# Kernel optimization log

Measured on AMD Instinct MI355X. Metric: run time of the kernel, lower is better.

The kernel has to match this reference:

```python
import jax, jax.numpy as jnp
import numpy as np
from math import sqrt


def setup_inputs() -> dict:
    key = jax.random.key(0)
    kq, kk, kv = jax.random.split(key, 3)
    B, L, H, E = 4, 2048, 8, 64
    S, D = L, E
    return {
        "queries": jax.random.normal(kq, (B, L, H, E), dtype=jnp.float32),
        "keys": jax.random.normal(kk, (B, S, H, E), dtype=jnp.float32),
        "values": jax.random.normal(kv, (B, S, H, D), dtype=jnp.float32),
    }


def reference(queries, keys, values):
    # FullAttention with mask_flag=True (TriangularCausalMask), dropout p=0,
    # output_attention=False. scale = 1/sqrt(E).
    B, L, H, E = queries.shape
    S = keys.shape[1]
    scale = 1.0 / sqrt(E)
    # scores: [B, H, L, S]
    scores = jnp.einsum("blhe,bshe->bhls", queries, keys)
    # causal mask: positions s > l are masked (upper triangle above diagonal)
    causal = jnp.tril(jnp.ones((L, S), dtype=bool))  # True = keep
    neg_inf = jnp.finfo(scores.dtype).min
    scores = jnp.where(causal, scores, neg_inf)
    A = jax.nn.softmax(scale * scores, axis=-1)  # [B,H,L,S]
    # context: [B, L, H, D]
    V = jnp.einsum("bhls,bshd->blhd", A, values)
    return V
```

## Files before the change

kernel.cpp:

```cpp
#include <hip/hip_runtime.h>
#include <math.h>

#define BD 4
#define LD 2048
#define HD 8
#define ED 64
#define TQ 64
#define TK 64
#define RS (HD * ED)

typedef __attribute__((ext_vector_type(8))) _Float16 f16x8;
typedef __attribute__((ext_vector_type(4))) _Float16 f16x4;
typedef __attribute__((ext_vector_type(4))) float f32x4;
typedef __attribute__((ext_vector_type(4))) unsigned int u32x4;
typedef __attribute__((ext_vector_type(2))) unsigned int u32x2;
typedef unsigned int u32;
typedef unsigned long long u64;

__device__ inline u32 pkh(float a, float b) {
    return __builtin_bit_cast(u32, __builtin_amdgcn_cvt_pkrtz(a, b));
}
__device__ inline u64 pkh4(float a, float b, float c, float d) {
    return (u64)pkh(a, b) | ((u64)pkh(c, d) << 32);
}
__device__ inline int swz(int row, int bcol) {
    return row * 128 + ((((bcol >> 4) ^ row) & 7) << 4) + (bcol & 15);
}

__global__ __launch_bounds__(256, 4)
void fa_mfma_q64(const float* __restrict__ Q, const float* __restrict__ K,
                 const float* __restrict__ V, float* __restrict__ O) {
    __shared__ __align__(16) char smem[32768];

    const int t    = threadIdx.x;
    const int lane = t & 63;
    const int w    = t >> 6;
    const int m16  = lane & 15;
    const int quad = lane >> 4;

    const int b = blockIdx.x >> 3;
    const int h = blockIdx.x & 7;
    const int y  = (int)blockIdx.y;
    const int r  = y & 7;
    const int c  = y >> 3;
    const int qt = (c == 0) ? (31 - r) : (c == 1) ? (r + 8)
                 : (c == 2) ? (23 - r) : r;
    const int q0  = qt * TQ;
    const int len = qt + 1;

    const int ks  = t >> 2;
    const int ke0 = (t & 3) << 2;
    const int vs0 = (t & 15) << 2;
    const int vd0 = (t >> 4) << 2;

    const float* Kbase = K + ((size_t)((b * LD + ks) * HD + h)) * ED + ke0;
    const float* Vbase = V + ((size_t)((b * LD + vs0) * HD + h)) * ED + vd0;

    const float qscale = 0.125f * 1.44269504088896340736f;
    f16x8 qf[2];
    {
        const float* qrow =
            Q + ((size_t)((b * LD + q0 + (w << 4) + m16) * HD + h)) * ED;
        #pragma unroll
        for (int hf = 0; hf < 2; ++hf) {
            const float4 x  = *(const float4*)(qrow + hf * 32 + quad * 8);
            const float4 y4 = *(const float4*)(qrow + hf * 32 + quad * 8 + 4);
            u32x4 p;
            p[0] = pkh(x.x * qscale, x.y * qscale);
            p[1] = pkh(x.z * qscale, x.w * qscale);
            p[2] = pkh(y4.x * qscale, y4.y * qscale);
            p[3] = pkh(y4.z * qscale, y4.w * qscale);
            qf[hf] = __builtin_bit_cast(f16x8, p);
        }
    }

    f32x4 oacc[4];
    float l_i = 0.0f;
    #pragma unroll
    for (int nt = 0; nt < 4; ++nt) oacc[nt] = (f32x4){0.f, 0.f, 0.f, 0.f};

    float4 kx[4], vx[4];
    {
        #pragma unroll
        for (int j = 0; j < 4; ++j) kx[j] = *(const float4*)(Kbase + 16 * j);
        #pragma unroll
        for (int rr = 0; rr < 4; ++rr) vx[rr] = *(const float4*)(Vbase + rr * RS);
        char* wK = smem;
        char* wV = smem + 16384;
        #pragma unroll
        for (int j = 0; j < 4; ++j)
            *(u64*)(wK + swz(ks, 2 * (ke0 + 16 * j))) = pkh4(kx[j].x, kx[j].y, kx[j].z, kx[j].w);
        *(u64*)(wV + swz(vd0 + 0, 2 * vs0)) = pkh4(vx[0].x, vx[1].x, vx[2].x, vx[3].x);
        *(u64*)(wV + swz(vd0 + 1, 2 * vs0)) = pkh4(vx[0].y, vx[1].y, vx[2].y, vx[3].y);
        *(u64*)(wV + swz(vd0 + 2, 2 * vs0)) = pkh4(vx[0].z, vx[1].z, vx[2].z, vx[3].z);
        *(u64*)(wV + swz(vd0 + 3, 2 * vs0)) = pkh4(vx[0].w, vx[1].w, vx[2].w, vx[3].w);
    }
    __syncthreads();

    for (int kt = 0; kt < len; ++kt) {
        char* rK = smem + ((kt & 1) << 13);
        char* rV = smem + 16384 + ((kt & 1) << 13);
        const bool pre = kt < len - 1;

        if (pre) {
            const float* kp = Kbase + (size_t)(kt + 1) * (TK * RS);
            const float* vp = Vbase + (size_t)(kt + 1) * (TK * RS);
            #pragma unroll
            for (int j = 0; j < 4; ++j) kx[j] = *(const float4*)(kp + 16 * j);
            #pragma unroll
            for (int rr = 0; rr < 4; ++rr) vx[rr] = *(const float4*)(vp + rr * RS);
        }

        f32x4 sacc[4];
        #pragma unroll
        for (int kc = 0; kc < 4; ++kc) {
            const f16x8 kf0 = *(const f16x8*)(rK + swz(kc * 16 + m16, quad * 16));
            const f16x8 kf1 = *(const f16x8*)(rK + swz(kc * 16 + m16, 64 + quad * 16));
            f32x4 z = {0.f, 0.f, 0.f, 0.f};
            z = __builtin_amdgcn_mfma_f32_16x16x32_f16(kf0, qf[0], z, 0, 0, 0);
            z = __builtin_amdgcn_mfma_f32_16x16x32_f16(kf1, qf[1], z, 0, 0, 0);
            sacc[kc] = z;
        }

        if (kt == qt) {
            const int ql = (w << 4) + m16;
            #pragma unroll
            for (int kc = 0; kc < 4; ++kc)
                #pragma unroll
                for (int i = 0; i < 4; ++i)
                    if (kc * 16 + quad * 4 + i > ql) sacc[kc][i] = -INFINITY;
        }

        f16x4 pf[4];
        #pragma unroll
        for (int kc = 0; kc < 4; ++kc) {
            float p0 = __builtin_amdgcn_exp2f(sacc[kc][0]);
            float p1 = __builtin_amdgcn_exp2f(sacc[kc][1]);
            float p2 = __builtin_amdgcn_exp2f(sacc[kc][2]);
            float p3 = __builtin_amdgcn_exp2f(sacc[kc][3]);
            l_i += (p0 + p1) + (p2 + p3);
            u32x2 pp;
            pp[0] = pkh(p0, p1);
            pp[1] = pkh(p2, p3);
            pf[kc] = __builtin_bit_cast(f16x4, pp);
        }

        #pragma unroll
        for (int kc = 0; kc < 4; ++kc) {
            #pragma unroll
            for (int dt = 0; dt < 4; ++dt) {
                const f16x4 vf = *(const f16x4*)
                    (rV + swz(dt * 16 + m16, 2 * (kc * 16 + quad * 4)));
                oacc[dt] = __builtin_amdgcn_mfma_f32_16x16x16f16(vf, pf[kc], oacc[dt], 0, 0, 0);
            }
        }

        if (pre) {
            char* wK = smem + ((kt & 1) ? 0 : 8192);
            char* wV = smem + 16384 + ((kt & 1) ? 0 : 8192);
            #pragma unroll
            for (int j = 0; j < 4; ++j)
                *(u64*)(wK + swz(ks, 2 * (ke0 + 16 * j))) = pkh4(kx[j].x, kx[j].y, kx[j].z, kx[j].w);
            *(u64*)(wV + swz(vd0 + 0, 2 * vs0)) = pkh4(vx[0].x, vx[1].x, vx[2].x, vx[3].x);
            *(u64*)(wV + swz(vd0 + 1, 2 * vs0)) = pkh4(vx[0].y, vx[1].y, vx[2].y, vx[3].y);
            *(u64*)(wV + swz(vd0 + 2, 2 * vs0)) = pkh4(vx[0].z, vx[1].z, vx[2].z, vx[3].z);
            *(u64*)(wV + swz(vd0 + 3, 2 * vs0)) = pkh4(vx[0].w, vx[1].w, vx[2].w, vx[3].w);
        }
        __syncthreads();
    }

    {
        float l = l_i;
        l += __shfl_xor(l, 16);
        l += __shfl_xor(l, 32);
        const float inv = 1.0f / l;
        float* orow =
            O + ((size_t)((b * LD + q0 + (w << 4) + m16) * HD + h)) * ED;
        #pragma unroll
        for (int dt = 0; dt < 4; ++dt) {
            float4 o;
            o.x = oacc[dt][0] * inv;
            o.y = oacc[dt][1] * inv;
            o.z = oacc[dt][2] * inv;
            o.w = oacc[dt][3] * inv;
            *(float4*)(orow + dt * 16 + quad * 4) = o;
        }
    }
}

extern "C" void kernel_launch(void* const* d_in, const int* in_sizes, int n_in,
                              void* d_out, int out_size, void* d_ws, size_t ws_size,
                              hipStream_t stream) {
    const float* Q = (const float*)d_in[0];
    const float* K = (const float*)d_in[1];
    const float* V = (const float*)d_in[2];
    float* O = (float*)d_out;
    dim3 grid(BD * HD, 32);
    fa_mfma_q64<<<grid, 256, 0, stream>>>(Q, K, V, O);
}
```

Baseline: 124.0 us.

## Fold paired causal query tiles into one block for balanced work

Each block now processes two query tiles, f and 31-f, back to back in a single 33-iteration key loop, so every block does the same amount of causal work. The grid is halved to 512 blocks, which removes tail imbalance and halves per-block launch and prologue costs. The trade-off is fewer blocks in flight on a large GPU and longer serial chains per block, plus mid-loop output writes and Q reloads. The kt sequence for the second tile runs backwards, so the diagonal mask is applied at its first tile.

```diff
diff --git a/kernel.cpp b/kernel.cpp
--- a/kernel.cpp
+++ b/kernel.cpp
@@ -28,8 +28,8 @@
 }
 
 __global__ __launch_bounds__(256, 4)
-void fa_mfma_q64(const float* __restrict__ Q, const float* __restrict__ K,
-                 const float* __restrict__ V, float* __restrict__ O) {
+void fa_mfma_fold(const float* __restrict__ Q, const float* __restrict__ K,
+                  const float* __restrict__ V, float* __restrict__ O) {
     __shared__ __align__(16) char smem[32768];
 
     const int t    = threadIdx.x;
@@ -40,13 +40,9 @@
 
     const int b = blockIdx.x >> 3;
     const int h = blockIdx.x & 7;
-    const int y  = (int)blockIdx.y;
-    const int r  = y & 7;
-    const int c  = y >> 3;
-    const int qt = (c == 0) ? (31 - r) : (c == 1) ? (r + 8)
-                 : (c == 2) ? (23 - r) : r;
-    const int q0  = qt * TQ;
-    const int len = qt + 1;
+    const int f = (int)blockIdx.y;
+    const int qtA = f;
+    const int qtB = 31 - f;
 
     const int ks  = t >> 2;
     const int ke0 = (t & 3) << 2;
@@ -60,7 +56,7 @@
     f16x8 qf[2];
     {
         const float* qrow =
-            Q + ((size_t)((b * LD + q0 + (w << 4) + m16) * HD + h)) * ED;
+            Q + ((size_t)((b * LD + qtA * TQ + (w << 4) + m16) * HD + h)) * ED;
         #pragma unroll
         for (int hf = 0; hf < 2; ++hf) {
             const float4 x  = *(const float4*)(qrow + hf * 32 + quad * 8);
@@ -97,14 +93,17 @@
     }
     __syncthreads();
 
-    for (int kt = 0; kt < len; ++kt) {
-        char* rK = smem + ((kt & 1) << 13);
-        char* rV = smem + 16384 + ((kt & 1) << 13);
-        const bool pre = kt < len - 1;
+    for (int i = 0; i < 33; ++i) {
+        const int kt = (i <= f) ? i : 32 - i;
+        const int qt = (i <= f) ? qtA : qtB;
+        char* rK = smem + ((i & 1) << 13);
+        char* rV = smem + 16384 + ((i & 1) << 13);
+        const bool pre = i < 32;
 
         if (pre) {
-            const float* kp = Kbase + (size_t)(kt + 1) * (TK * RS);
-            const float* vp = Vbase + (size_t)(kt + 1) * (TK * RS);
+            const int ktn = (i < f) ? (i + 1) : (31 - i);
+            const float* kp = Kbase + (size_t)ktn * (TK * RS);
+            const float* vp = Vbase + (size_t)ktn * (TK * RS);
             #pragma unroll
             for (int j = 0; j < 4; ++j) kx[j] = *(const float4*)(kp + 16 * j);
             #pragma unroll
@@ -127,8 +126,8 @@
             #pragma unroll
             for (int kc = 0; kc < 4; ++kc)
                 #pragma unroll
-                for (int i = 0; i < 4; ++i)
-                    if (kc * 16 + quad * 4 + i > ql) sacc[kc][i] = -INFINITY;
+                for (int ii = 0; ii < 4; ++ii)
+                    if (kc * 16 + quad * 4 + ii > ql) sacc[kc][ii] = -INFINITY;
         }
 
         f16x4 pf[4];
@@ -155,9 +154,42 @@
             }
         }
 
+        if (i == f) {
+            float l = l_i;
+            l += __shfl_xor(l, 16);
+            l += __shfl_xor(l, 32);
+            const float inv = 1.0f / l;
+            float* orow =
+                O + ((size_t)((b * LD + qtA * TQ + (w << 4) + m16) * HD + h)) * ED;
+            #pragma unroll
+            for (int dt = 0; dt < 4; ++dt) {
+                float4 o;
+                o.x = oacc[dt][0] * inv;
+                o.y = oacc[dt][1] * inv;
+                o.z = oacc[dt][2] * inv;
+                o.w = oacc[dt][3] * inv;
+                *(float4*)(orow + dt * 16 + quad * 4) = o;
+                oacc[dt] = (f32x4){0.f, 0.f, 0.f, 0.f};
+            }
+            l_i = 0.0f;
+            const float* qrow =
+                Q + ((size_t)((b * LD + qtB * TQ + (w << 4) + m16) * HD + h)) * ED;
+            #pragma unroll
+            for (int hf = 0; hf < 2; ++hf) {
+                const float4 x  = *(const float4*)(qrow + hf * 32 + quad * 8);
+                const float4 y4 = *(const float4*)(qrow + hf * 32 + quad * 8 + 4);
+                u32x4 p;
+                p[0] = pkh(x.x * qscale, x.y * qscale);
+                p[1] = pkh(x.z * qscale, x.w * qscale);
+                p[2] = pkh(y4.x * qscale, y4.y * qscale);
+                p[3] = pkh(y4.z * qscale, y4.w * qscale);
+                qf[hf] = __builtin_bit_cast(f16x8, p);
+            }
+        }
+
         if (pre) {
-            char* wK = smem + ((kt & 1) ? 0 : 8192);
-            char* wV = smem + 16384 + ((kt & 1) ? 0 : 8192);
+            char* wK = smem + ((i & 1) ? 0 : 8192);
+            char* wV = smem + 16384 + ((i & 1) ? 0 : 8192);
             #pragma unroll
             for (int j = 0; j < 4; ++j)
                 *(u64*)(wK + swz(ks, 2 * (ke0 + 16 * j))) = pkh4(kx[j].x, kx[j].y, kx[j].z, kx[j].w);
@@ -175,7 +207,7 @@
         l += __shfl_xor(l, 32);
         const float inv = 1.0f / l;
         float* orow =
-            O + ((size_t)((b * LD + q0 + (w << 4) + m16) * HD + h)) * ED;
+            O + ((size_t)((b * LD + qtB * TQ + (w << 4) + m16) * HD + h)) * ED;
         #pragma unroll
         for (int dt = 0; dt < 4; ++dt) {
             float4 o;
@@ -195,6 +227,6 @@
     const float* K = (const float*)d_in[1];
     const float* V = (const float*)d_in[2];
     float* O = (float*)d_out;
-    dim3 grid(BD * HD, 32);
-    fa_mfma_q64<<<grid, 256, 0, stream>>>(Q, K, V, O);
-}
+    dim3 grid(BD * HD, 16);
+    fa_mfma_fold<<<grid, 256, 0, stream>>>(Q, K, V, O);
+}
```

New measurement: 128.1 us. 3.3% more time.

## Precompute swizzled fp16 K/V tiles and stream them via global_load_lds

Applied to the files above, without the earlier changes.

Adds a pre-pass kernel that converts K and V to fp16 once, in the final swizzled/transposed LDS layout, and stores them in workspace. The attention kernel then copies those tiles straight into LDS with global_load_lds, with no per-block fp32 loads, conversion or LDS stores. This removes the redundant conversion that every query-tile block repeated and halves the bytes read per K/V tile. The cost is an extra launch plus a workspace round trip. The old path remains as a fallback when the workspace is too small.

```diff
diff --git a/kernel.cpp b/kernel.cpp
--- a/kernel.cpp
+++ b/kernel.cpp
@@ -8,6 +8,8 @@
 #define TQ 64
 #define TK 64
 #define RS (HD * ED)
+#define NT 32
+#define TILE_BYTES 8192
 
 typedef __attribute__((ext_vector_type(8))) _Float16 f16x8;
 typedef __attribute__((ext_vector_type(4))) _Float16 f16x4;
@@ -26,10 +28,50 @@
 __device__ inline int swz(int row, int bcol) {
     return row * 128 + ((((bcol >> 4) ^ row) & 7) << 4) + (bcol & 15);
 }
+__device__ __forceinline__ void gload_lds16(const char* g, char* l) {
+    __builtin_amdgcn_global_load_lds(
+        (const __attribute__((address_space(1))) unsigned int*)g,
+        (__attribute__((address_space(3))) unsigned int*)l, 16, 0, 0);
+}
 
 __global__ __launch_bounds__(256, 4)
-void fa_mfma_q64(const float* __restrict__ Q, const float* __restrict__ K,
-                 const float* __restrict__ V, float* __restrict__ O) {
+void cvt_kv(const float* __restrict__ K, const float* __restrict__ V,
+            char* __restrict__ Kimg, char* __restrict__ Vimg) {
+    const int t  = threadIdx.x;
+    const int b  = blockIdx.x >> 3;
+    const int h  = blockIdx.x & 7;
+    const int kt = blockIdx.y;
+
+    const int ks  = t >> 2;
+    const int ke0 = (t & 3) << 2;
+    const int vs0 = (t & 15) << 2;
+    const int vd0 = (t >> 4) << 2;
+
+    const size_t tb = ((size_t)((b * HD + h) * NT + kt)) * TILE_BYTES;
+    char* kd = Kimg + tb;
+    char* vd = Vimg + tb;
+
+    const float* kp = K + ((size_t)((b * LD + kt * TK + ks) * HD + h)) * ED + ke0;
+    const float* vp = V + ((size_t)((b * LD + kt * TK + vs0) * HD + h)) * ED + vd0;
+
+    float4 kx[4], vx[4];
+    #pragma unroll
+    for (int j = 0; j < 4; ++j) kx[j] = *(const float4*)(kp + 16 * j);
+    #pragma unroll
+    for (int r = 0; r < 4; ++r) vx[r] = *(const float4*)(vp + r * RS);
+
+    #pragma unroll
+    for (int j = 0; j < 4; ++j)
+        *(u64*)(kd + swz(ks, 2 * (ke0 + 16 * j))) = pkh4(kx[j].x, kx[j].y, kx[j].z, kx[j].w);
+    *(u64*)(vd + swz(vd0 + 0, 2 * vs0)) = pkh4(vx[0].x, vx[1].x, vx[2].x, vx[3].x);
+    *(u64*)(vd + swz(vd0 + 1, 2 * vs0)) = pkh4(vx[0].y, vx[1].y, vx[2].y, vx[3].y);
+    *(u64*)(vd + swz(vd0 + 2, 2 * vs0)) = pkh4(vx[0].z, vx[1].z, vx[2].z, vx[3].z);
+    *(u64*)(vd + swz(vd0 + 3, 2 * vs0)) = pkh4(vx[0].w, vx[1].w, vx[2].w, vx[3].w);
+}
+
+__global__ __launch_bounds__(256, 4)
+void fa_f16img(const char* __restrict__ Kimg, const char* __restrict__ Vimg,
+               const float* __restrict__ Q, float* __restrict__ O) {
     __shared__ __align__(16) char smem[32768];
 
     const int t    = threadIdx.x;
@@ -48,13 +90,10 @@
     const int q0  = qt * TQ;
     const int len = qt + 1;
 
-    const int ks  = t >> 2;
-    const int ke0 = (t & 3) << 2;
-    const int vs0 = (t & 15) << 2;
-    const int vd0 = (t >> 4) << 2;
-
-    const float* Kbase = K + ((size_t)((b * LD + ks) * HD + h)) * ED + ke0;
-    const float* Vbase = V + ((size_t)((b * LD + vs0) * HD + h)) * ED + vd0;
+    const char* Kt = Kimg + (size_t)(b * HD + h) * NT * TILE_BYTES;
+    const char* Vt = Vimg + (size_t)(b * HD + h) * NT * TILE_BYTES;
+    const int lsrc = (w << 10) + (lane << 4);
+    const int ldst = (w << 10);
 
     const float qscale = 0.125f * 1.44269504088896340736f;
     f16x8 qf[2];
@@ -79,36 +118,30 @@
     #pragma unroll
     for (int nt = 0; nt < 4; ++nt) oacc[nt] = (f32x4){0.f, 0.f, 0.f, 0.f};
 
-    float4 kx[4], vx[4];
-    {
-        #pragma unroll
-        for (int j = 0; j < 4; ++j) kx[j] = *(const float4*)(Kbase + 16 * j);
-        #pragma unroll
-        for (int rr = 0; rr < 4; ++rr) vx[rr] = *(const float4*)(Vbase + rr * RS);
-        char* wK = smem;
-        char* wV = smem + 16384;
-        #pragma unroll
-        for (int j = 0; j < 4; ++j)
-            *(u64*)(wK + swz(ks, 2 * (ke0 + 16 * j))) = pkh4(kx[j].x, kx[j].y, kx[j].z, kx[j].w);
-        *(u64*)(wV + swz(vd0 + 0, 2 * vs0)) = pkh4(vx[0].x, vx[1].x, vx[2].x, vx[3].x);
-        *(u64*)(wV + swz(vd0 + 1, 2 * vs0)) = pkh4(vx[0].y, vx[1].y, vx[2].y, vx[3].y);
-        *(u64*)(wV + swz(vd0 + 2, 2 * vs0)) = pkh4(vx[0].z, vx[1].z, vx[2].z, vx[3].z);
-        *(u64*)(wV + swz(vd0 + 3, 2 * vs0)) = pkh4(vx[0].w, vx[1].w, vx[2].w, vx[3].w);
+    {
+        const char* ks = Kt;
+        const char* vs = Vt;
+        #pragma unroll
+        for (int inst = 0; inst < 2; ++inst) {
+            gload_lds16(ks + inst * 4096 + lsrc, smem + inst * 4096 + ldst);
+            gload_lds16(vs + inst * 4096 + lsrc, smem + 16384 + inst * 4096 + ldst);
+        }
     }
     __syncthreads();
 
     for (int kt = 0; kt < len; ++kt) {
         char* rK = smem + ((kt & 1) << 13);
         char* rV = smem + 16384 + ((kt & 1) << 13);
-        const bool pre = kt < len - 1;
-
-        if (pre) {
-            const float* kp = Kbase + (size_t)(kt + 1) * (TK * RS);
-            const float* vp = Vbase + (size_t)(kt + 1) * (TK * RS);
-            #pragma unroll
-            for (int j = 0; j < 4; ++j) kx[j] = *(const float4*)(kp + 16 * j);
-            #pragma unroll
-            for (int rr = 0; rr < 4; ++rr) vx[rr] = *(const float4*)(vp + rr * RS);
+
+        if (kt < len - 1) {
+            const char* ks = Kt + (size_t)(kt + 1) * TILE_BYTES;
+            const char* vs = Vt + (size_t)(kt + 1) * TILE_BYTES;
+            const int bo = ((kt & 1) ^ 1) << 13;
+            #pragma unroll
+            for (int inst = 0; inst < 2; ++inst) {
+                gload_lds16(ks + inst * 4096 + lsrc, smem + bo + inst * 4096 + ldst);
+                gload_lds16(vs + inst * 4096 + lsrc, smem + 16384 + bo + inst * 4096 + ldst);
+            }
         }
 
         f32x4 sacc[4];
@@ -155,17 +188,6 @@
             }
         }
 
-        if (pre) {
-            char* wK = smem + ((kt & 1) ? 0 : 8192);
-            char* wV = smem + 16384 + ((kt & 1) ? 0 : 8192);
-            #pragma unroll
-            for (int j = 0; j < 4; ++j)
-                *(u64*)(wK + swz(ks, 2 * (ke0 + 16 * j))) = pkh4(kx[j].x, kx[j].y, kx[j].z, kx[j].w);
-            *(u64*)(wV + swz(vd0 + 0, 2 * vs0)) = pkh4(vx[0].x, vx[1].x, vx[2].x, vx[3].x);
-            *(u64*)(wV + swz(vd0 + 1, 2 * vs0)) = pkh4(vx[0].y, vx[1].y, vx[2].y, vx[3].y);
-            *(u64*)(wV + swz(vd0 + 2, 2 * vs0)) = pkh4(vx[0].z, vx[1].z, vx[2].z, vx[3].z);
-            *(u64*)(wV + swz(vd0 + 3, 2 * vs0)) = pkh4(vx[0].w, vx[1].w, vx[2].w, vx[3].w);
-        }
         __syncthreads();
     }
 
@@ -188,6 +210,141 @@
     }
 }
 
+__global__ __launch_bounds__(256, 4)
+void fa_mfma_q64(const float* __restrict__ Q, const float* __restrict__ K,
+                 const float* __restrict__ V, float* __restrict__ O) {
+    __shared__ __align__(16) char smem[32768];
+    const int t = threadIdx.x, lane = t & 63, w = t >> 6;
+    const int m16 = lane & 15, quad = lane >> 4;
+    const int b = blockIdx.x >> 3, h = blockIdx.x & 7;
+    const int y = (int)blockIdx.y, r = y & 7, c = y >> 3;
+    const int qt = (c == 0) ? (31 - r) : (c == 1) ? (r + 8) : (c == 2) ? (23 - r) : r;
+    const int q0 = qt * TQ;
+    const int len = qt + 1;
+    const int ks = t >> 2, ke0 = (t & 3) << 2;
+    const int vs0 = (t & 15) << 2, vd0 = (t >> 4) << 2;
+    const float* Kbase = K + ((size_t)((b * LD + ks) * HD + h)) * ED + ke0;
+    const float* Vbase = V + ((size_t)((b * LD + vs0) * HD + h)) * ED + vd0;
+    const float qscale = 0.125f * 1.44269504088896340736f;
+    f16x8 qf[2];
+    {
+        const float* qrow = Q + ((size_t)((b * LD + q0 + (w << 4) + m16) * HD + h)) * ED;
+        #pragma unroll
+        for (int hf = 0; hf < 2; ++hf) {
+            const float4 x = *(const float4*)(qrow + hf * 32 + quad * 8);
+            const float4 y4 = *(const float4*)(qrow + hf * 32 + quad * 8 + 4);
+            u32x4 p;
+            p[0] = pkh(x.x * qscale, x.y * qscale);
+            p[1] = pkh(x.z * qscale, x.w * qscale);
+            p[2] = pkh(y4.x * qscale, y4.y * qscale);
+            p[3] = pkh(y4.z * qscale, y4.w * qscale);
+            qf[hf] = __builtin_bit_cast(f16x8, p);
+        }
+    }
+    f32x4 oacc[4];
+    float l_i = 0.0f;
+    #pragma unroll
+    for (int nt = 0; nt < 4; ++nt) oacc[nt] = (f32x4){0.f, 0.f, 0.f, 0.f};
+    float4 kx[4], vx[4];
+    {
+        #pragma unroll
+        for (int j = 0; j < 4; ++j) kx[j] = *(const float4*)(Kbase + 16 * j);
+        #pragma unroll
+        for (int rr = 0; rr < 4; ++rr) vx[rr] = *(const float4*)(Vbase + rr * RS);
+        char* wK = smem;
+        char* wV = smem + 16384;
+        #pragma unroll
+        for (int j = 0; j < 4; ++j)
+            *(u64*)(wK + swz(ks, 2 * (ke0 + 16 * j))) = pkh4(kx[j].x, kx[j].y, kx[j].z, kx[j].w);
+        *(u64*)(wV + swz(vd0 + 0, 2 * vs0)) = pkh4(vx[0].x, vx[1].x, vx[2].x, vx[3].x);
+        *(u64*)(wV + swz(vd0 + 1, 2 * vs0)) = pkh4(vx[0].y, vx[1].y, vx[2].y, vx[3].y);
+        *(u64*)(wV + swz(vd0 + 2, 2 * vs0)) = pkh4(vx[0].z, vx[1].z, vx[2].z, vx[3].z);
+        *(u64*)(wV + swz(vd0 + 3, 2 * vs0)) = pkh4(vx[0].w, vx[1].w, vx[2].w, vx[3].w);
+    }
+    __syncthreads();
+    for (int kt = 0; kt < len; ++kt) {
+        char* rK = smem + ((kt & 1) << 13);
+        char* rV = smem + 16384 + ((kt & 1) << 13);
+        const bool pre = kt < len - 1;
+        if (pre) {
+            const float* kp = Kbase + (size_t)(kt + 1) * (TK * RS);
+            const float* vp = Vbase + (size_t)(kt + 1) * (TK * RS);
+            #pragma unroll
+            for (int j = 0; j < 4; ++j) kx[j] = *(const float4*)(kp + 16 * j);
+            #pragma unroll
+            for (int rr = 0; rr < 4; ++rr) vx[rr] = *(const float4*)(vp + rr * RS);
+        }
+        f32x4 sacc[4];
+        #pragma unroll
+        for (int kc = 0; kc < 4; ++kc) {
+            const f16x8 kf0 = *(const f16x8*)(rK + swz(kc * 16 + m16, quad * 16));
+            const f16x8 kf1 = *(const f16x8*)(rK + swz(kc * 16 + m16, 64 + quad * 16));
+            f32x4 z = {0.f, 0.f, 0.f, 0.f};
+            z = __builtin_amdgcn_mfma_f32_16x16x32_f16(kf0, qf[0], z, 0, 0, 0);
+            z = __builtin_amdgcn_mfma_f32_16x16x32_f16(kf1, qf[1], z, 0, 0, 0);
+            sacc[kc] = z;
+        }
+        if (kt == qt) {
+            const int ql = (w << 4) + m16;
+            #pragma unroll
+            for (int kc = 0; kc < 4; ++kc)
+                #pragma unroll
+                for (int i = 0; i < 4; ++i)
+                    if (kc * 16 + quad * 4 + i > ql) sacc[kc][i] = -INFINITY;
+        }
+        f16x4 pf[4];
+        #pragma unroll
+        for (int kc = 0; kc < 4; ++kc) {
+            float p0 = __builtin_amdgcn_exp2f(sacc[kc][0]);
+            float p1 = __builtin_amdgcn_exp2f(sacc[kc][1]);
+            float p2 = __builtin_amdgcn_exp2f(sacc[kc][2]);
+            float p3 = __builtin_amdgcn_exp2f(sacc[kc][3]);
+            l_i += (p0 + p1) + (p2 + p3);
+            u32x2 pp;
+            pp[0] = pkh(p0, p1);
+            pp[1] = pkh(p2, p3);
+            pf[kc] = __builtin_bit_cast(f16x4, pp);
+        }
+        #pragma unroll
+        for (int kc = 0; kc < 4; ++kc) {
+            #pragma unroll
+            for (int dt = 0; dt < 4; ++dt) {
+                const f16x4 vf = *(const f16x4*)
+                    (rV + swz(dt * 16 + m16, 2 * (kc * 16 + quad * 4)));
+                oacc[dt] = __builtin_amdgcn_mfma_f32_16x16x16f16(vf, pf[kc], oacc[dt], 0, 0, 0);
+            }
+        }
+        if (pre) {
+            char* wK = smem + ((kt & 1) ? 0 : 8192);
+            char* wV = smem + 16384 + ((kt & 1) ? 0 : 8192);
+            #pragma unroll
+            for (int j = 0; j < 4; ++j)
+                *(u64*)(wK + swz(ks, 2 * (ke0 + 16 * j))) = pkh4(kx[j].x, kx[j].y, kx[j].z, kx[j].w);
+            *(u64*)(wV + swz(vd0 + 0, 2 * vs0)) = pkh4(vx[0].x, vx[1].x, vx[2].x, vx[3].x);
+            *(u64*)(wV + swz(vd0 + 1, 2 * vs0)) = pkh4(vx[0].y, vx[1].y, vx[2].y, vx[3].y);
+            *(u64*)(wV + swz(vd0 + 2, 2 * vs0)) = pkh4(vx[0].z, vx[1].z, vx[2].z, vx[3].z);
+            *(u64*)(wV + swz(vd0 + 3, 2 * vs0)) = pkh4(vx[0].w, vx[1].w, vx[2].w, vx[3].w);
+        }
+        __syncthreads();
+    }
+    {
+        float l = l_i;
+        l += __shfl_xor(l, 16);
+        l += __shfl_xor(l, 32);
+        const float inv = 1.0f / l;
+        float* orow = O + ((size_t)((b * LD + q0 + (w << 4) + m16) * HD + h)) * ED;
+        #pragma unroll
+        for (int dt = 0; dt < 4; ++dt) {
+            float4 o;
+            o.x = oacc[dt][0] * inv;
+            o.y = oacc[dt][1] * inv;
+            o.z = oacc[dt][2] * inv;
+            o.w = oacc[dt][3] * inv;
+            *(float4*)(orow + dt * 16 + quad * 4) = o;
+        }
+    }
+}
+
 extern "C" void kernel_launch(void* const* d_in, const int* in_sizes, int n_in,
                               void* d_out, int out_size, void* d_ws, size_t ws_size,
                               hipStream_t stream) {
@@ -195,6 +352,14 @@
     const float* K = (const float*)d_in[1];
     const float* V = (const float*)d_in[2];
     float* O = (float*)d_out;
-    dim3 grid(BD * HD, 32);
-    fa_mfma_q64<<<grid, 256, 0, stream>>>(Q, K, V, O);
-}
+
+    const size_t img = (size_t)BD * HD * NT * TILE_BYTES;
+    if (d_ws != nullptr && ws_size >= 2 * img) {
+        char* Kimg = (char*)d_ws;
+        char* Vimg = (char*)d_ws + img;
+        cvt_kv<<<dim3(BD * HD, NT), 256, 0, stream>>>(K, V, Kimg, Vimg);
+        fa_f16img<<<dim3(BD * HD, 32), 256, 0, stream>>>(Kimg, Vimg, Q, O);
+    } else {
+        fa_mfma_q64<<<dim3(BD * HD, 32), 256, 0, stream>>>(Q, K, V, O);
+    }
+}
```

After: 120.0 us. 3.3% less time.
